# Kernel optimization log

Hardware: AMD Instinct MI355X
Metric: run time of the kernel (lower is better)

Reference implementation:

```python
import jax, jax.numpy as jnp
import numpy as np

H, W = 160, 160
FS = 7
SPAN = FS // 2
NUM_CLASSES = 19
NUM_ITERS = 5
THETA_ALPHA = 160.0  # scales rgb in bilateral features
THETA_BETA = 3.0     # scales position in bilateral features
THETA_GAMMA = 3.0    # scales position in spatial features
EPS = 1e-20

# offsets ordered (dx outer, dy inner) to match TF filter-tap index (dx+span)*FS + (dy+span)
OFFSETS = [(dx, dy) for dx in range(-SPAN, SPAN + 1) for dy in range(-SPAN, SPAN + 1)]


def _make_filter(features):
    # features: (bs, cf, H, W) -> gaussian affinity filter (bs, FS*FS, H, W)
    # filter[b, k, i, j] = exp(-0.5 * ||f[b,:,i+dx,j+dy] - f[b,:,i,j]||^2), 0 if out of bounds
    fp = jnp.pad(features, ((0, 0), (0, 0), (SPAN, SPAN), (SPAN, SPAN)))
    rows = jnp.arange(H)
    cols = jnp.arange(W)
    taps = []
    for dx, dy in OFFSETS:
        shifted = fp[:, :, SPAN + dx:SPAN + dx + H, SPAN + dy:SPAN + dy + W]
        aff = jnp.exp(-0.5 * jnp.sum((features - shifted) ** 2, axis=1))  # (bs, H, W)
        mask = (((rows + dx >= 0) & (rows + dx < H))[:, None]
                & ((cols + dy >= 0) & (cols + dy < W))[None, :])
        taps.append(aff * mask)
    return jnp.stack(taps, axis=1)  # (bs, FS*FS, H, W)


def _patches(x):
    # x: (bs, C, H, W) -> (bs, C, FS*FS, H, W), zero-padded shifts (matches extract_patches SAME)
    xp = jnp.pad(x, ((0, 0), (0, 0), (SPAN, SPAN), (SPAN, SPAN)))
    return jnp.stack(
        [xp[:, :, SPAN + dx:SPAN + dx + H, SPAN + dy:SPAN + dy + W] for dx, dy in OFFSETS],
        axis=2)


def _compute_gaussian(x, filt):
    # x: (bs, C, H, W), filt: (bs, FS*FS, H, W) -> (bs, C, H, W)
    return jnp.sum(_patches(x) * filt[:, None], axis=2)


def _forward(unaries, rgb, spatial_ker_weights, bilateral_ker_weights, compatibility_matrix):
    u = jnp.transpose(unaries, (0, 3, 1, 2))     # (bs, C, H, W)
    rgb_nchw = jnp.transpose(rgb, (0, 3, 1, 2))  # (bs, 3, H, W)
    bs = u.shape[0]
    mesh = jnp.stack(
        jnp.meshgrid(jnp.arange(H, dtype=jnp.float32), jnp.arange(W, dtype=jnp.float32),
                     indexing='ij'), 0)          # (2, H, W)
    spatial_feat = jnp.broadcast_to((mesh / THETA_GAMMA)[None], (bs, 2, H, W))
    bilateral_feat = jnp.concatenate(
        [rgb_nchw / THETA_ALPHA,
         jnp.broadcast_to((mesh / THETA_BETA)[None], (bs, 2, H, W))], axis=1)  # (bs, 5, H, W)

    spatial_filter = _make_filter(spatial_feat)
    bilateral_filter = _make_filter(bilateral_feat)

    ones = jnp.ones_like(u)
    spatial_norm = _compute_gaussian(ones, spatial_filter)
    bilateral_norm = _compute_gaussian(ones, bilateral_filter)

    q = u
    for _ in range(NUM_ITERS):
        # NOTE: original code does tf.nn.softmax(q_values, 0) -> softmax over the BATCH axis.
        sm = jax.nn.softmax(q, axis=0)
        s_out = _compute_gaussian(sm, spatial_filter) / (spatial_norm + EPS)
        b_out = _compute_gaussian(sm, bilateral_filter) / (bilateral_norm + EPS)
        msg = (jnp.einsum('kc,bchw->bkhw', spatial_ker_weights, s_out)
               + jnp.einsum('kc,bchw->bkhw', bilateral_ker_weights, b_out))
        pairwise = jnp.einsum('kc,bchw->bkhw', compatibility_matrix, msg)
        q = u - pairwise
    return jnp.transpose(q, (0, 2, 3, 1))  # (bs, H, W, C)


def setup_inputs() -> dict:
    key = jax.random.key(0)
    k1, k2 = jax.random.split(key)
    unaries = jax.random.normal(k1, (2, H, W, NUM_CLASSES), dtype=jnp.float32)
    rgb = jax.random.uniform(k2, (2, H, W, 3), dtype=jnp.float32) * 255.0
    eye = jnp.eye(NUM_CLASSES, dtype=jnp.float32)
    return {
        'unaries': unaries,
        'rgb': rgb,
        'spatial_ker_weights': eye,            # _diagonal_initializer
        'bilateral_ker_weights': eye,          # _diagonal_initializer
        'compatibility_matrix': -eye,          # _potts_model_initializer
    }


def reference(unaries, rgb, spatial_ker_weights, bilateral_ker_weights, compatibility_matrix):
    return _forward(unaries, rgb, spatial_ker_weights, bilateral_ker_weights,
                    compatibility_matrix)
```

## Files before the change

### kernel.cpp

```cpp
#include <hip/hip_runtime.h>


typedef __attribute__((ext_vector_type(4))) _Float16 half4;
typedef __attribute__((ext_vector_type(2))) _Float16 half2f;
typedef __attribute__((ext_vector_type(4))) float float4v;

#define HH 160
#define WW 160
#define NPIX (HH*WW)
#define NC 19
#define NG 5
#define SPAN 3
#define TR 10
#define TC 10
#define NPXT 100
#define LR 16
#define LC 16
#define LCP 18
#define HSTRIDE (LR*LCP)
#define NHALO (LR*LC)
#define NRING 156
#define NBLK 256
#define NTHR 512
#define NACT 500
#define EPSF 1e-20f

#define EPTAG   0x5EED0000u
#define EPMASK  0xFFFF0000u

#define EPW(b) (32 + (b)*32)

#define SZ_A    24064
#define PN_OFF  9216
#define OFF_WB  SZ_A
#define SHM_SZ  (SZ_A + 20000)

__device__ __forceinline__ float fast_rcp(float x) { return __builtin_amdgcn_rcpf(x); }

__device__ __forceinline__ float smx0(float q0, float q1) {
    const float m  = fmaxf(q0, q1);
    const float e0 = __expf(q0 - m);
    const float e1 = __expf(q1 - m);
    return e0 * fast_rcp(e0 + e1);
}

__device__ __forceinline__ unsigned ep_decode(unsigned w) {
    return ((w & EPMASK) == EPTAG) ? (w & 0xFFFFu) : 0u;
}

__global__ void __launch_bounds__(NTHR) crf_kernel(
        const float* __restrict__ u,
        const float* __restrict__ rgb,
        const float* __restrict__ sw,
        const float* __restrict__ bw,
        const float* __restrict__ compat,
        unsigned long long* __restrict__ gsmA,
        unsigned long long* __restrict__ gsmB,
        unsigned* __restrict__ bar,
        float* __restrict__ out) {
    __shared__ __align__(16) char shm[SHM_SZ];
    __shared__ float Msh[960];
    __shared__ float rowsum[NC];
    __shared__ int   diagflag;
    float4*   rgbL = (float4*)shm;
    float4v*  smF  = (float4v*)shm;
    float*    accF = (float*)shm;
    unsigned* wbW  = (unsigned*)(shm + OFF_WB);
    const uint2* wbP = (const uint2*)(shm + OFF_WB);

    constexpr float WSPC[49] = {
        0.36787944f,0.48567179f,0.57375342f,0.60653066f,0.57375342f,0.48567179f,0.36787944f,
        0.48567179f,0.64118039f,0.75746513f,0.80073740f,0.75746513f,0.64118039f,0.48567179f,
        0.57375342f,0.75746513f,0.89483932f,0.94595947f,0.89483932f,0.75746513f,0.57375342f,
        0.60653066f,0.80073740f,0.94595947f,1.00000000f,0.94595947f,0.80073740f,0.60653066f,
        0.57375342f,0.75746513f,0.89483932f,0.94595947f,0.89483932f,0.75746513f,0.57375342f,
        0.48567179f,0.64118039f,0.75746513f,0.80073740f,0.75746513f,0.64118039f,0.48567179f,
        0.36787944f,0.48567179f,0.57375342f,0.60653066f,0.57375342f,0.48567179f,0.36787944f };

    const int tid = threadIdx.x;
    const bool act = (tid < NACT);
    const int g   = tid / NPXT;
    const int px  = tid - g * NPXT;
    const int r   = px / TC, c = px - r * TC;
    const int ti0 = blockIdx.y * TR, tj0 = blockIdx.x * TC;
    const int gp  = (ti0 + r) * WW + (tj0 + c);
    const int ctr = (r + SPAN) * LCP + (c + SPAN);
    const int ku  = 4 * g;
    const int bid = blockIdx.y * 16 + blockIdx.x;

    int nb[8];
    {
        const int bx = blockIdx.x, by = blockIdx.y;
        int k = 0;
        #pragma unroll
        for (int dy2 = -1; dy2 <= 1; ++dy2)
            #pragma unroll
            for (int dx2 = -1; dx2 <= 1; ++dx2) {
                if (dx2 == 0 && dy2 == 0) continue;
                const int nx = bx + dx2, ny = by + dy2;
                nb[k++] = ((unsigned)nx < 16u && (unsigned)ny < 16u) ? (ny*16 + nx) : bid;
            }
    }

    if (tid == 0) diagflag = 1;

    float uv0[4], uv1[4];
    half4 sh;
    float smv[4];
    if (act) {
        #pragma unroll
        for (int i = 0; i < 4; ++i) {
            const int ch = 4*g + i;
            uv0[i] = (ch < NC) ? u[(size_t)gp * NC + ch] : 0.0f;
            uv1[i] = (ch < NC) ? u[((size_t)NPIX + gp) * NC + ch] : 0.0f;
        }
        #pragma unroll
        for (int i = 0; i < 4; ++i) {
            smv[i] = smx0(uv0[i], uv1[i]);
            sh[i]  = (_Float16)smv[i];
        }
        unsigned long long u64; __builtin_memcpy(&u64, &sh, 8);
        __hip_atomic_store(&gsmA[g * NPIX + gp], u64,
                           __ATOMIC_RELAXED, __HIP_MEMORY_SCOPE_AGENT);
    }

    if (tid < NC) {
        float rs = 0.0f;
        for (int cb = 0; cb < NC; ++cb) rs += sw[tid*NC + cb] + bw[tid*NC + cb];
        rowsum[tid] = rs;
    }
    __syncthreads();
    if (tid == 0)
        __hip_atomic_store(&bar[EPW(bid)], EPTAG | 1u,
                           __ATOMIC_RELAXED, __HIP_MEMORY_SCOPE_AGENT);

    float4 rv;
    int rgb_idx;
    {
        const int bb = tid >> 8, pos = tid & 255;
        const int hr = pos >> 4, hc = pos & 15;
        const int yi = ti0 - SPAN + hr, xj = tj0 - SPAN + hc;
        rv = make_float4(0.f, 0.f, 0.f, 0.f);
        if ((unsigned)yi < HH && (unsigned)xj < WW) {
            const float* p = rgb + ((size_t)(bb * NPIX) + yi * WW + xj) * 3;
            rv = make_float4(p[0]*(1.f/160.f), p[1]*(1.f/160.f), p[2]*(1.f/160.f), 1.f);
        }
        rgb_idx = bb * HSTRIDE + hr * LCP + hc;
    }

    for (int e = tid; e < 960; e += NTHR) {
        const int k = e / 48, cc2 = e % 48;
        float acc = 0.0f;
        if (k < NC) {
            if (cc2 < NC) {
                for (int j = 0; j < NC; ++j) acc += compat[k*NC + j] * sw[j*NC + cc2];
            } else if (cc2 >= 20 && cc2 < 20 + NC) {
                const int cb = cc2 - 20;
                for (int j = 0; j < NC; ++j) acc += compat[k*NC + j] * bw[j*NC + cb];
            } else if (cc2 == 40) {
                for (int j = 0; j < NC; ++j) acc += compat[k*NC + j] * rowsum[j];
            }
        }
        Msh[e] = acc;
        bool off = false;
        if (k < NC) {
            if (cc2 < NC && cc2 != k && acc != 0.0f) off = true;
            if (cc2 >= 20 && cc2 < 20 + NC && (cc2 - 20) != k && acc != 0.0f) off = true;
        }
        if (off) atomicAnd(&diagflag, 0);
    }

    rgbL[rgb_idx] = rv;
    __syncthreads();

    float dsv[4], dbv[4];
    #pragma unroll
    for (int i = 0; i < 4; ++i) {
        dsv[i] = Msh[(ku + i) * 48 + (ku + i)];
        dbv[i] = Msh[(ku + i) * 48 + 20 + (ku + i)];
    }
    const bool isdiag = (diagflag != 0);

    if (act) {
        const float4 cv0 = rgbL[ctr];
        const float4 cv1 = rgbL[HSTRIDE + ctr];
        const int tapb = g * 10;
        const int ntap = (g == 4) ? 9 : 10;
        float pn0 = 0.f, pn1 = 0.f;
        for (int i = 0; i < ntap; ++i) {
            const int t = tapb + i;
            const int dx = t / 7 - SPAN, dy = t % 7 - SPAN;
            const int n = ctr + dx * LCP + dy;
            const float4 nv0 = rgbL[n];
            const float4 nv1 = rgbL[HSTRIDE + n];
            const float spc = (float)(dx*dx + dy*dy) * (-1.f/18.f);
            const float dr0 = cv0.x-nv0.x, dg0 = cv0.y-nv0.y, db0 = cv0.z-nv0.z;
            const float dr1 = cv1.x-nv1.x, dg1 = cv1.y-nv1.y, db1 = cv1.z-nv1.z;
            const float d0 = dr0*dr0 + dg0*dg0 + db0*db0;
            const float d1 = dr1*dr1 + dg1*dg1 + db1*db1;
            const float wb0 = nv0.w * __expf(fmaf(d0, -0.5f, spc));
            const float wb1 = nv0.w * __expf(fmaf(d1, -0.5f, spc));
            half2f hw = {(_Float16)wb0, (_Float16)wb1};
            unsigned uw; __builtin_memcpy(&uw, &hw, 4);
            wbW[(t >> 1) * 200 + px * 2 + (t & 1)] = uw;
            pn0 += (float)hw.x; pn1 += (float)hw.y;
        }
        if (g == 4) wbW[24 * 200 + px * 2 + 1] = 0u;
        *(float2*)(shm + PN_OFF + (g * NPXT + px) * 8) = make_float2(pn0, pn1);
    }
    __syncthreads();

    float snI, bnI0, bnI1;
    if (act) {
        float bn0 = 0.f, bn1 = 0.f;
        #pragma unroll
        for (int g2 = 0; g2 < 5; ++g2) {
            const float2 p = *(const float2*)(shm + PN_OFF + (g2 * NPXT + px) * 8);
            bn0 += p.x; bn1 += p.y;
        }
        const int rg = ti0 + r, cg = tj0 + c;
        float Rr = 5.70645506f, Cc = 5.70645506f;
        Rr -= (rg < 3   ? 0.60653066f : 0.f) + (rg < 2   ? 0.80073740f : 0.f)
            + (rg < 1   ? 0.94595947f : 0.f) + (rg > 156 ? 0.60653066f : 0.f)
            + (rg > 157 ? 0.80073740f : 0.f) + (rg > 158 ? 0.94595947f : 0.f);
        Cc -= (cg < 3   ? 0.60653066f : 0.f) + (cg < 2   ? 0.80073740f : 0.f)
            + (cg < 1   ? 0.94595947f : 0.f) + (cg > 156 ? 0.60653066f : 0.f)
            + (cg > 157 ? 0.80073740f : 0.f) + (cg > 158 ? 0.94595947f : 0.f);
        snI  = fast_rcp(Rr * Cc + EPSF);
        bnI0 = fast_rcp(bn0 + EPSF);
        bnI1 = fast_rcp(bn1 + EPSF);
    }

    for (int it = 0; it < 5; ++it) {
        __syncthreads();

        if (act) {
            const float4v sv = {smv[0], smv[1], smv[2], smv[3]};
            smF[g * HSTRIDE + ctr] = sv;
        }

        if (tid == 0) {
            const unsigned seq = (unsigned)(it + 1);
            if (it > 0)
                __hip_atomic_store(&bar[EPW(bid)], EPTAG | seq,
                                   __ATOMIC_RELAXED, __HIP_MEMORY_SCOPE_AGENT);
            unsigned mn;
            unsigned spins = 0;
            do {
                mn = 0xFFFFu;
                #pragma unroll
                for (int k = 0; k < 8; ++k) {
                    const unsigned w = __hip_atomic_load(&bar[EPW(nb[k])],
                                                         __ATOMIC_RELAXED, __HIP_MEMORY_SCOPE_AGENT);
                    const unsigned e = ep_decode(w);
                    mn = (e < mn) ? e : mn;
                }
                if (mn < seq) {
                    __builtin_amdgcn_s_sleep(1);
                    if (++spins > (1u << 22)) break;
                }
            } while (mn < seq);
        }
        __syncthreads();

        const unsigned long long* gsrc = ((it & 1) ? gsmB : gsmA);
        #pragma unroll
        for (int k2 = 0; k2 < 2; ++k2) {
            const int e = tid + NTHR * k2;
            if (e < NG * NRING) {
                const int sg = e / NRING, re = e - sg * NRING;
                int hr, hc;
                if (re < 48)        { hr = re >> 4;               hc = re & 15; }
                else if (re < 96)   { hr = 13 + ((re - 48) >> 4); hc = (re - 48) & 15; }
                else                { const int t2 = re - 96; hr = 3 + t2 / 6;
                                      const int s = t2 % 6;   hc = (s < 3) ? s : s + 10; }
                const int yi = ti0 - SPAN + hr, xj = tj0 - SPAN + hc;
                float4v fv = (float4v)0.0f;
                if ((unsigned)yi < HH && (unsigned)xj < WW) {
                    const unsigned long long raw =
                        __hip_atomic_load(&gsrc[sg * NPIX + yi * WW + xj],
                                          __ATOMIC_RELAXED, __HIP_MEMORY_SCOPE_AGENT);
                    half4 hv; __builtin_memcpy(&hv, &raw, 8);
                    fv = (float4v){(float)hv[0], (float)hv[1], (float)hv[2], (float)hv[3]};
                }
                smF[sg * HSTRIDE + hr * LCP + hc] = fv;
            }
        }
        __syncthreads();

        float4v sAv = (float4v)0.0f, b0a = (float4v)0.0f, b1a = (float4v)0.0f;
        if (act) {
            const float4v* pl = smF + g * HSTRIDE;
            #pragma unroll
            for (int i = 0; i < 24; ++i) {
                const uint2 wp = wbP[i * 100 + px];
                #pragma unroll
                for (int s = 0; s < 2; ++s) {
                    const int t = 2*i + s;
                    const int dx = t / 7 - SPAN, dy = t % 7 - SPAN;
                    half2f hw; __builtin_memcpy(&hw, s ? &wp.y : &wp.x, 4);
                    const float w0 = (float)hw.x, w1 = (float)hw.y;
                    const float4v f = pl[ctr + dx*LCP + dy];
                    sAv += WSPC[t] * f;
                    b0a += w0 * f;
                    b1a += w1 * f;
                }
            }
            {
                const uint2 wp = wbP[24 * 100 + px];
                half2f hw; __builtin_memcpy(&hw, &wp.x, 4);
                const float w0 = (float)hw.x, w1 = (float)hw.y;
                const float4v f = pl[ctr + SPAN*LCP + SPAN];
                sAv += WSPC[48] * f;
                b0a += w0 * f;
                b1a += w1 * f;
            }
        }

        float q0v[4], q1v[4];
        if (isdiag) {
            if (act) {
                #pragma unroll
                for (int i = 0; i < 4; ++i) {
                    const float sAn = sAv[i] * snI;
                    const float b0n = b0a[i] * bnI0;
                    const float b1x = b1a[i] * bnI1;
                    q0v[i] = uv0[i] - dsv[i]*sAn - dbv[i]*b0n;
                    q1v[i] = uv1[i] - (dsv[i] + dbv[i]) + dsv[i]*sAn + dbv[i]*b1x;
                }
            }
        } else {
            __syncthreads();
            if (act) {
                #pragma unroll
                for (int i = 0; i < 4; ++i) {
                    accF[(4*g + i) * NPXT + px]      = sAv[i] * snI;
                    accF[(20 + 4*g + i) * NPXT + px] = b0a[i] * bnI0;
                    accF[(40 + 4*g + i) * NPXT + px] = b1a[i] * bnI1;
                }
            }
            __syncthreads();
            if (act) {
                float t1[4] = {0,0,0,0}, t2[4] = {0,0,0,0}, t3[4] = {0,0,0,0};
                #pragma unroll
                for (int cc = 0; cc < 20; ++cc) {
                    const float sv  = accF[cc * NPXT + px];
                    const float b0v = accF[(20 + cc) * NPXT + px];
                    const float b1v = accF[(40 + cc) * NPXT + px];
                    #pragma unroll
                    for (int i = 0; i < 4; ++i) {
                        const float* mk = Msh + (ku + i) * 48;
                        t1[i] += mk[cc] * sv;
                        t2[i] += mk[20 + cc] * b0v;
                        t3[i] += mk[20 + cc] * b1v;
                    }
                }
                #pragma unroll
                for (int i = 0; i < 4; ++i) {
                    const float rs = Msh[(ku + i) * 48 + 40];
                    q0v[i] = uv0[i] - t1[i] - t2[i];
                    q1v[i] = uv1[i] - rs + t1[i] + t3[i];
                }
            }
        }

        if (it == 4) {
            if (act) {
                #pragma unroll
                for (int i = 0; i < 4; ++i) {
                    const int ch = 4*g + i;
                    if (ch < NC) {
                        out[(size_t)gp * NC + ch]          = q0v[i];
                        out[((size_t)NPIX + gp) * NC + ch] = q1v[i];
                    }
                }
            }
        } else if (act) {
            #pragma unroll
            for (int i = 0; i < 4; ++i) {
                smv[i] = smx0(q0v[i], q1v[i]);
                sh[i]  = (_Float16)smv[i];
            }
            unsigned long long u64; __builtin_memcpy(&u64, &sh, 8);
            unsigned long long* gdst = (((it + 1) & 1) ? gsmB : gsmA);
            __hip_atomic_store(&gdst[g * NPIX + gp], u64,
                               __ATOMIC_RELAXED, __HIP_MEMORY_SCOPE_AGENT);
        }
    }
}

extern "C" void kernel_launch(void* const* d_in, const int* in_sizes, int n_in,
                              void* d_out, int out_size, void* d_ws, size_t ws_size,
                              hipStream_t stream) {
    const float* u      = (const float*)d_in[0];
    const float* rgb    = (const float*)d_in[1];
    const float* sw     = (const float*)d_in[2];
    const float* bw     = (const float*)d_in[3];
    const float* compat = (const float*)d_in[4];
    float* out = (float*)d_out;

    unsigned long long* gsmA = (unsigned long long*)d_ws;
    unsigned long long* gsmB = (unsigned long long*)((char*)d_ws + 1024000);
    unsigned* bar = (unsigned*)((char*)d_ws + 2048000);

    crf_kernel<<<dim3(WW/TC, HH/TR, 1), dim3(NTHR), 0, stream>>>(
        u, rgb, sw, bw, compat, gsmA, gsmB, bar, out);
}
```

Measured before the change: 95.90 us.

## Split channels into ten groups of two and double threads per block

The block grows from 512 to 1024 threads, and each thread now handles 2 channels instead of 4. The per-thread channel vectors become float2, and the global softmax exchange uses 32-bit half2 words. Bilateral weights are now kept as fp32 pairs in LDS instead of packed fp16, which raises the LDS footprint to about 72KB. The aim is to cut per-thread serial work and register pressure on the 49-tap loop, at the cost of more LDS traffic and heavier block barriers.

```diff
diff --git a/kernel.cpp b/kernel.cpp
--- a/kernel.cpp
+++ b/kernel.cpp
@@ -1,39 +1,36 @@
 #include <hip/hip_runtime.h>
 
 
-typedef __attribute__((ext_vector_type(4))) _Float16 half4;
 typedef __attribute__((ext_vector_type(2))) _Float16 half2f;
-typedef __attribute__((ext_vector_type(4))) float float4v;
+typedef __attribute__((ext_vector_type(2))) float float2v;
 
 #define HH 160
 #define WW 160
 #define NPIX (HH*WW)
 #define NC 19
-#define NG 5
+#define NG 10
 #define SPAN 3
 #define TR 10
 #define TC 10
 #define NPXT 100
 #define LR 16
 #define LC 16
-#define LCP 18
-#define HSTRIDE (LR*LCP)
-#define NHALO (LR*LC)
+#define LCP2 26
+#define PSTRIDE (LR*LCP2)
+#define LCP4 18
+#define HSTR4 (LR*LCP4)
 #define NRING 156
-#define NBLK 256
-#define NTHR 512
-#define NACT 500
+#define NTHR 1024
+#define NACT 1000
 #define EPSF 1e-20f
 
 #define EPTAG   0x5EED0000u
 #define EPMASK  0xFFFF0000u
-
-#define EPW(b) (32 + (b)*32)
-
-#define SZ_A    24064
+#define EPW(b)  (32 + (b)*32)
+
 #define PN_OFF  9216
-#define OFF_WB  SZ_A
-#define SHM_SZ  (SZ_A + 20000)
+#define OFF_WB  33280
+#define SHM_SZ  72480
 
 __device__ __forceinline__ float fast_rcp(float x) { return __builtin_amdgcn_rcpf(x); }
 
@@ -54,8 +51,8 @@
         const float* __restrict__ sw,
         const float* __restrict__ bw,
         const float* __restrict__ compat,
-        unsigned long long* __restrict__ gsmA,
-        unsigned long long* __restrict__ gsmB,
+        unsigned* __restrict__ gsmA,
+        unsigned* __restrict__ gsmB,
         unsigned* __restrict__ bar,
         float* __restrict__ out) {
     __shared__ __align__(16) char shm[SHM_SZ];
@@ -63,10 +60,9 @@
     __shared__ float rowsum[NC];
     __shared__ int   diagflag;
     float4*   rgbL = (float4*)shm;
-    float4v*  smF  = (float4v*)shm;
+    float2v*  smP  = (float2v*)shm;
     float*    accF = (float*)shm;
-    unsigned* wbW  = (unsigned*)(shm + OFF_WB);
-    const uint2* wbP = (const uint2*)(shm + OFF_WB);
+    float2v*  wbF  = (float2v*)(shm + OFF_WB);
 
     constexpr float WSPC[49] = {
         0.36787944f,0.48567179f,0.57375342f,0.60653066f,0.57375342f,0.48567179f,0.36787944f,
@@ -84,8 +80,8 @@
     const int r   = px / TC, c = px - r * TC;
     const int ti0 = blockIdx.y * TR, tj0 = blockIdx.x * TC;
     const int gp  = (ti0 + r) * WW + (tj0 + c);
-    const int ctr = (r + SPAN) * LCP + (c + SPAN);
-    const int ku  = 4 * g;
+    const int ctr2 = (r + SPAN) * LCP2 + (c + SPAN);
+    const int ctr4 = (r + SPAN) * LCP4 + (c + SPAN);
     const int bid = blockIdx.y * 16 + blockIdx.x;
 
     int nb[8];
@@ -104,23 +100,19 @@
 
     if (tid == 0) diagflag = 1;
 
-    float uv0[4], uv1[4];
-    half4 sh;
-    float smv[4];
+    float uv0[2], uv1[2];
+    float smv[2];
     if (act) {
         #pragma unroll
-        for (int i = 0; i < 4; ++i) {
-            const int ch = 4*g + i;
+        for (int i = 0; i < 2; ++i) {
+            const int ch = 2*g + i;
             uv0[i] = (ch < NC) ? u[(size_t)gp * NC + ch] : 0.0f;
             uv1[i] = (ch < NC) ? u[((size_t)NPIX + gp) * NC + ch] : 0.0f;
-        }
-        #pragma unroll
-        for (int i = 0; i < 4; ++i) {
             smv[i] = smx0(uv0[i], uv1[i]);
-            sh[i]  = (_Float16)smv[i];
-        }
-        unsigned long long u64; __builtin_memcpy(&u64, &sh, 8);
-        __hip_atomic_store(&gsmA[g * NPIX + gp], u64,
+        }
+        half2f hp = {(_Float16)smv[0], (_Float16)smv[1]};
+        unsigned u32; __builtin_memcpy(&u32, &hp, 4);
+        __hip_atomic_store(&gsmA[g * NPIX + gp], u32,
                            __ATOMIC_RELAXED, __HIP_MEMORY_SCOPE_AGENT);
     }
 
@@ -135,8 +127,8 @@
                            __ATOMIC_RELAXED, __HIP_MEMORY_SCOPE_AGENT);
 
     float4 rv;
-    int rgb_idx;
-    {
+    int rgb_idx = -1;
+    if (tid < 512) {
         const int bb = tid >> 8, pos = tid & 255;
         const int hr = pos >> 4, hc = pos & 15;
         const int yi = ti0 - SPAN + hr, xj = tj0 - SPAN + hc;
@@ -145,7 +137,7 @@
             const float* p = rgb + ((size_t)(bb * NPIX) + yi * WW + xj) * 3;
             rv = make_float4(p[0]*(1.f/160.f), p[1]*(1.f/160.f), p[2]*(1.f/160.f), 1.f);
         }
-        rgb_idx = bb * HSTRIDE + hr * LCP + hc;
+        rgb_idx = bb * HSTR4 + hr * LCP4 + hc;
     }
 
     for (int e = tid; e < 960; e += NTHR) {
@@ -170,29 +162,32 @@
         if (off) atomicAnd(&diagflag, 0);
     }
 
-    rgbL[rgb_idx] = rv;
+    if (rgb_idx >= 0) rgbL[rgb_idx] = rv;
     __syncthreads();
 
-    float dsv[4], dbv[4];
-    #pragma unroll
-    for (int i = 0; i < 4; ++i) {
-        dsv[i] = Msh[(ku + i) * 48 + (ku + i)];
-        dbv[i] = Msh[(ku + i) * 48 + 20 + (ku + i)];
+    float dsv[2], dbv[2];
+    if (act) {
+        #pragma unroll
+        for (int i = 0; i < 2; ++i) {
+            const int k = 2*g + i;
+            dsv[i] = Msh[k * 48 + k];
+            dbv[i] = Msh[k * 48 + 20 + k];
+        }
     }
     const bool isdiag = (diagflag != 0);
 
     if (act) {
-        const float4 cv0 = rgbL[ctr];
-        const float4 cv1 = rgbL[HSTRIDE + ctr];
-        const int tapb = g * 10;
-        const int ntap = (g == 4) ? 9 : 10;
+        const float4 cv0 = rgbL[ctr4];
+        const float4 cv1 = rgbL[HSTR4 + ctr4];
+        const int tb = 5 * g;
+        const int ntap = (g == 9) ? 4 : 5;
         float pn0 = 0.f, pn1 = 0.f;
         for (int i = 0; i < ntap; ++i) {
-            const int t = tapb + i;
+            const int t = tb + i;
             const int dx = t / 7 - SPAN, dy = t % 7 - SPAN;
-            const int n = ctr + dx * LCP + dy;
+            const int n = ctr4 + dx * LCP4 + dy;
             const float4 nv0 = rgbL[n];
-            const float4 nv1 = rgbL[HSTRIDE + n];
+            const float4 nv1 = rgbL[HSTR4 + n];
             const float spc = (float)(dx*dx + dy*dy) * (-1.f/18.f);
             const float dr0 = cv0.x-nv0.x, dg0 = cv0.y-nv0.y, db0 = cv0.z-nv0.z;
             const float dr1 = cv1.x-nv1.x, dg1 = cv1.y-nv1.y, db1 = cv1.z-nv1.z;
@@ -200,12 +195,9 @@
             const float d1 = dr1*dr1 + dg1*dg1 + db1*db1;
             const float wb0 = nv0.w * __expf(fmaf(d0, -0.5f, spc));
             const float wb1 = nv0.w * __expf(fmaf(d1, -0.5f, spc));
-            half2f hw = {(_Float16)wb0, (_Float16)wb1};
-            unsigned uw; __builtin_memcpy(&uw, &hw, 4);
-            wbW[(t >> 1) * 200 + px * 2 + (t & 1)] = uw;
-            pn0 += (float)hw.x; pn1 += (float)hw.y;
-        }
-        if (g == 4) wbW[24 * 200 + px * 2 + 1] = 0u;
+            wbF[t * NPXT + px] = (float2v){wb0, wb1};
+            pn0 += wb0; pn1 += wb1;
+        }
         *(float2*)(shm + PN_OFF + (g * NPXT + px) * 8) = make_float2(pn0, pn1);
     }
     __syncthreads();
@@ -214,7 +206,7 @@
     if (act) {
         float bn0 = 0.f, bn1 = 0.f;
         #pragma unroll
-        for (int g2 = 0; g2 < 5; ++g2) {
+        for (int g2 = 0; g2 < NG; ++g2) {
             const float2 p = *(const float2*)(shm + PN_OFF + (g2 * NPXT + px) * 8);
             bn0 += p.x; bn1 += p.y;
         }
@@ -234,10 +226,7 @@
     for (int it = 0; it < 5; ++it) {
         __syncthreads();
 
-        if (act) {
-            const float4v sv = {smv[0], smv[1], smv[2], smv[3]};
-            smF[g * HSTRIDE + ctr] = sv;
-        }
+        if (act) smP[g * PSTRIDE + ctr2] = (float2v){smv[0], smv[1]};
 
         if (tid == 0) {
             const unsigned seq = (unsigned)(it + 1);
@@ -263,7 +252,7 @@
         }
         __syncthreads();
 
-        const unsigned long long* gsrc = ((it & 1) ? gsmB : gsmA);
+        const unsigned* gsrc = ((it & 1) ? gsmB : gsmA);
         #pragma unroll
         for (int k2 = 0; k2 < 2; ++k2) {
             const int e = tid + NTHR * k2;
@@ -275,53 +264,41 @@
                 else                { const int t2 = re - 96; hr = 3 + t2 / 6;
                                       const int s = t2 % 6;   hc = (s < 3) ? s : s + 10; }
                 const int yi = ti0 - SPAN + hr, xj = tj0 - SPAN + hc;
-                float4v fv = (float4v)0.0f;
+                float2v fv = (float2v){0.f, 0.f};
                 if ((unsigned)yi < HH && (unsigned)xj < WW) {
-                    const unsigned long long raw =
+                    const unsigned raw =
                         __hip_atomic_load(&gsrc[sg * NPIX + yi * WW + xj],
                                           __ATOMIC_RELAXED, __HIP_MEMORY_SCOPE_AGENT);
-                    half4 hv; __builtin_memcpy(&hv, &raw, 8);
-                    fv = (float4v){(float)hv[0], (float)hv[1], (float)hv[2], (float)hv[3]};
-                }
-                smF[sg * HSTRIDE + hr * LCP + hc] = fv;
+                    half2f hv; __builtin_memcpy(&hv, &raw, 4);
+                    fv = (float2v){(float)hv.x, (float)hv.y};
+                }
+                smP[sg * PSTRIDE + hr * LCP2 + hc] = fv;
             }
         }
         __syncthreads();
 
-        float4v sAv = (float4v)0.0f, b0a = (float4v)0.0f, b1a = (float4v)0.0f;
+        float2v sA2 = (float2v){0.f,0.f}, b02 = (float2v){0.f,0.f}, b12 = (float2v){0.f,0.f};
         if (act) {
-            const float4v* pl = smF + g * HSTRIDE;
+            const float2v* pl = smP + g * PSTRIDE + ctr2;
             #pragma unroll
-            for (int i = 0; i < 24; ++i) {
-                const uint2 wp = wbP[i * 100 + px];
-                #pragma unroll
-                for (int s = 0; s < 2; ++s) {
-                    const int t = 2*i + s;
-                    const int dx = t / 7 - SPAN, dy = t % 7 - SPAN;
-                    half2f hw; __builtin_memcpy(&hw, s ? &wp.y : &wp.x, 4);
-                    const float w0 = (float)hw.x, w1 = (float)hw.y;
-                    const float4v f = pl[ctr + dx*LCP + dy];
-                    sAv += WSPC[t] * f;
-                    b0a += w0 * f;
-                    b1a += w1 * f;
-                }
-            }
-            {
-                const uint2 wp = wbP[24 * 100 + px];
-                half2f hw; __builtin_memcpy(&hw, &wp.x, 4);
-                const float w0 = (float)hw.x, w1 = (float)hw.y;
-                const float4v f = pl[ctr + SPAN*LCP + SPAN];
-                sAv += WSPC[48] * f;
-                b0a += w0 * f;
-                b1a += w1 * f;
-            }
-        }
-
-        float q0v[4], q1v[4];
+            for (int t = 0; t < 49; ++t) {
+                const int dx = t / 7 - SPAN, dy = t % 7 - SPAN;
+                const float2v f = pl[dx * LCP2 + dy];
+                const float2v w = wbF[t * NPXT + px];
+                sA2 += WSPC[t] * f;
+                b02 += w.x * f;
+                b12 += w.y * f;
+            }
+        }
+        const float sAv[2] = {sA2.x, sA2.y};
+        const float b0a[2] = {b02.x, b02.y};
+        const float b1a[2] = {b12.x, b12.y};
+
+        float q0v[2], q1v[2];
         if (isdiag) {
             if (act) {
                 #pragma unroll
-                for (int i = 0; i < 4; ++i) {
+                for (int i = 0; i < 2; ++i) {
                     const float sAn = sAv[i] * snI;
                     const float b0n = b0a[i] * bnI0;
                     const float b1x = b1a[i] * bnI1;
@@ -333,31 +310,31 @@
             __syncthreads();
             if (act) {
                 #pragma unroll
-                for (int i = 0; i < 4; ++i) {
-                    accF[(4*g + i) * NPXT + px]      = sAv[i] * snI;
-                    accF[(20 + 4*g + i) * NPXT + px] = b0a[i] * bnI0;
-                    accF[(40 + 4*g + i) * NPXT + px] = b1a[i] * bnI1;
+                for (int i = 0; i < 2; ++i) {
+                    accF[(2*g + i) * NPXT + px]      = sAv[i] * snI;
+                    accF[(20 + 2*g + i) * NPXT + px] = b0a[i] * bnI0;
+                    accF[(40 + 2*g + i) * NPXT + px] = b1a[i] * bnI1;
                 }
             }
             __syncthreads();
             if (act) {
-                float t1[4] = {0,0,0,0}, t2[4] = {0,0,0,0}, t3[4] = {0,0,0,0};
+                float t1[2] = {0,0}, t2[2] = {0,0}, t3[2] = {0,0};
                 #pragma unroll
                 for (int cc = 0; cc < 20; ++cc) {
                     const float sv  = accF[cc * NPXT + px];
                     const float b0v = accF[(20 + cc) * NPXT + px];
                     const float b1v = accF[(40 + cc) * NPXT + px];
                     #pragma unroll
-                    for (int i = 0; i < 4; ++i) {
-                        const float* mk = Msh + (ku + i) * 48;
+                    for (int i = 0; i < 2; ++i) {
+                        const float* mk = Msh + (2*g + i) * 48;
                         t1[i] += mk[cc] * sv;
                         t2[i] += mk[20 + cc] * b0v;
                         t3[i] += mk[20 + cc] * b1v;
                     }
                 }
                 #pragma unroll
-                for (int i = 0; i < 4; ++i) {
-                    const float rs = Msh[(ku + i) * 48 + 40];
+                for (int i = 0; i < 2; ++i) {
+                    const float rs = Msh[(2*g + i) * 48 + 40];
                     q0v[i] = uv0[i] - t1[i] - t2[i];
                     q1v[i] = uv1[i] - rs + t1[i] + t3[i];
                 }
@@ -367,8 +344,8 @@
         if (it == 4) {
             if (act) {
                 #pragma unroll
-                for (int i = 0; i < 4; ++i) {
-                    const int ch = 4*g + i;
+                for (int i = 0; i < 2; ++i) {
+                    const int ch = 2*g + i;
                     if (ch < NC) {
                         out[(size_t)gp * NC + ch]          = q0v[i];
                         out[((size_t)NPIX + gp) * NC + ch] = q1v[i];
@@ -377,13 +354,11 @@
             }
         } else if (act) {
             #pragma unroll
-            for (int i = 0; i < 4; ++i) {
-                smv[i] = smx0(q0v[i], q1v[i]);
-                sh[i]  = (_Float16)smv[i];
-            }
-            unsigned long long u64; __builtin_memcpy(&u64, &sh, 8);
-            unsigned long long* gdst = (((it + 1) & 1) ? gsmB : gsmA);
-            __hip_atomic_store(&gdst[g * NPIX + gp], u64,
+            for (int i = 0; i < 2; ++i) smv[i] = smx0(q0v[i], q1v[i]);
+            half2f hp = {(_Float16)smv[0], (_Float16)smv[1]};
+            unsigned u32; __builtin_memcpy(&u32, &hp, 4);
+            unsigned* gdst = (((it + 1) & 1) ? gsmB : gsmA);
+            __hip_atomic_store(&gdst[g * NPIX + gp], u32,
                                __ATOMIC_RELAXED, __HIP_MEMORY_SCOPE_AGENT);
         }
     }
@@ -399,9 +374,9 @@
     const float* compat = (const float*)d_in[4];
     float* out = (float*)d_out;
 
-    unsigned long long* gsmA = (unsigned long long*)d_ws;
-    unsigned long long* gsmB = (unsigned long long*)((char*)d_ws + 1024000);
-    unsigned* bar = (unsigned*)((char*)d_ws + 2048000);
+    unsigned* gsmA = (unsigned*)d_ws;
+    unsigned* gsmB = (unsigned*)((char*)d_ws + 1024000);
+    unsigned* bar  = (unsigned*)((char*)d_ws + 2048000);
 
     crf_kernel<<<dim3(WW/TC, HH/TR, 1), dim3(NTHR), 0, stream>>>(
         u, rgb, sw, bw, compat, gsmA, gsmB, bar, out);
```

New measurement: 100.7 us. 1.05x slower.
